# Kernel tuning notes

Hardware: AMD Instinct MI355X
Metric: run time of the kernel (lower is better)

The kernel has to match this reference:

```python
import jax, jax.numpy as jnp
import numpy as np

NH, KVH, HD = 32, 8, 128          # num heads, kv heads, head dim
HIDDEN = NH * HD                   # 4096
K_BITS = V_BITS = 4
GROUP = 32                         # quantization group size
THETA = 10000.0
FEAT = 32 // K_BITS                # values packed per int32


def _rope_cos_sin(pos, dtype=jnp.float32):
    inv_freq = 1.0 / (THETA ** (jnp.arange(0, HD, 2, dtype=jnp.float32) / HD))
    freqs = pos.astype(jnp.float32)[:, None] * inv_freq[None, :]
    emb = jnp.concatenate([freqs, freqs], axis=-1)  # [t, HD]
    return jnp.cos(emb).astype(dtype), jnp.sin(emb).astype(dtype)


def _rotate_half(x):
    x1, x2 = jnp.split(x, 2, axis=-1)
    return jnp.concatenate([-x2, x1], axis=-1)


def _apply_rope(x, pos):  # x: [b, h, t, d], pos: [t]
    cos, sin = _rope_cos_sin(pos, x.dtype)
    return x * cos[None, None] + _rotate_half(x) * sin[None, None]


def _unpack(packed, bits):
    # packed int32 [..., n] -> float [..., n * (32//bits)], little-endian bit fields
    feat = 32 // bits
    shifts = jnp.arange(feat, dtype=jnp.int32) * bits
    vals = (packed[..., None] >> shifts) & ((1 << bits) - 1)
    return vals.reshape(packed.shape[:-1] + (packed.shape[-1] * feat,)).astype(jnp.float32)


def _dequant(packed, scale, mn, bits, group):
    # group-wise affine dequant: x = q * scale + mn along last dim
    qv = _unpack(packed, bits)
    lead, L = qv.shape[:-1], qv.shape[-1]
    qv = qv.reshape(lead + (L // group, group))
    return (qv * scale[..., None] + mn[..., None]).reshape(lead + (L,))


def _repeat_kv(x, n):
    return jnp.repeat(x, n, axis=1)


def setup_inputs() -> dict:
    key = jax.random.key(0)
    ks = jax.random.split(key, 13)
    B, QL = 8, 8
    TQ, FULL_PAST = 3968, 56
    s = 0.02
    return {
        "hidden_states": jax.random.normal(ks[0], (B, QL, HIDDEN), jnp.float32),
        "Wq": jax.random.normal(ks[1], (NH * HD, HIDDEN), jnp.float32) * s,
        "Wk": jax.random.normal(ks[2], (KVH * HD, HIDDEN), jnp.float32) * s,
        "Wv": jax.random.normal(ks[3], (KVH * HD, HIDDEN), jnp.float32) * s,
        "Wo": jax.random.normal(ks[4], (NH * HD, NH * HD), jnp.float32) * s,
        "key_quant_trans": jax.random.randint(ks[5], (B, KVH, HD, TQ // FEAT), 0, 2**31 - 1, jnp.int32),
        "key_scale_trans": jax.random.uniform(ks[6], (B, KVH, HD, TQ // GROUP), jnp.float32) * 0.05 + 0.01,
        "key_mn_trans": jax.random.normal(ks[7], (B, KVH, HD, TQ // GROUP), jnp.float32) * 0.1,
        "key_full_past": jax.random.normal(ks[8], (B, KVH, FULL_PAST, HD), jnp.float32),
        "value_quant": jax.random.randint(ks[9], (B, KVH, TQ, HD // FEAT), 0, 2**31 - 1, jnp.int32),
        "value_scale": jax.random.uniform(ks[10], (B, KVH, TQ, HD // GROUP), jnp.float32) * 0.05 + 0.01,
        "value_mn": jax.random.normal(ks[11], (B, KVH, TQ, HD // GROUP), jnp.float32) * 0.1,
        "value_full_past": jax.random.normal(ks[12], (B, KVH, FULL_PAST, HD), jnp.float32),
    }


def reference(hidden_states, Wq, Wk, Wv, Wo,
              key_quant_trans, key_scale_trans, key_mn_trans, key_full_past,
              value_quant, value_scale, value_mn, value_full_past):
    b, q_len, _ = hidden_states.shape
    groups = NH // KVH
    # projections
    q = (hidden_states @ Wq.T).reshape(b, q_len, NH, HD).transpose(0, 2, 1, 3)
    k = (hidden_states @ Wk.T).reshape(b, q_len, KVH, HD).transpose(0, 2, 1, 3)
    v = (hidden_states @ Wv.T).reshape(b, q_len, KVH, HD).transpose(0, 2, 1, 3)

    TQ = key_quant_trans.shape[-1] * FEAT
    past_len = TQ + key_full_past.shape[2]
    pos_new = jnp.arange(past_len, past_len + q_len)
    qr = _apply_rope(q, pos_new)

    # quantized key segment: dequant (stored transposed [b,kvh,HD,TQ]) + fused RoPE + bmm
    kq = _dequant(key_quant_trans, key_scale_trans, key_mn_trans, K_BITS, GROUP)
    kq = _apply_rope(kq.transpose(0, 1, 3, 2), jnp.arange(TQ))  # [b,kvh,TQ,HD]
    att_quant = jnp.einsum('bhqd,bhkd->bhqk', qr, _repeat_kv(kq, groups))

    # full-precision residual key segment
    k_full = jnp.concatenate([key_full_past, k], axis=2)
    pos_full = jnp.arange(past_len + q_len - k_full.shape[2], past_len + q_len)
    k_full = _apply_rope(k_full, pos_full)
    att_full = jnp.einsum('bhqd,bhkd->bhqk', qr, _repeat_kv(k_full, groups))

    attn = jnp.concatenate([att_quant, att_full], axis=-1) / np.sqrt(HD).astype(np.float32)
    attn = jax.nn.softmax(attn.astype(jnp.float32), axis=-1).astype(qr.dtype)

    # quantized values (packed along head_dim) + full residual values
    vq = _dequant(value_quant, value_scale, value_mn, V_BITS, GROUP)  # [b,kvh,TQ,HD]
    v_full = jnp.concatenate([value_full_past, v], axis=2)
    Lf = v_full.shape[2]
    out = jnp.einsum('bhqk,bhkd->bhqd', attn[..., :-Lf], _repeat_kv(vq, groups)) \
        + jnp.einsum('bhqk,bhkd->bhqd', attn[..., -Lf:], _repeat_kv(v_full, groups))

    out = out.transpose(0, 2, 1, 3).reshape(b, q_len, NH * HD)
    return out @ Wo.T
```

## Files before the change

kernel.cpp:

```cpp
#include <hip/hip_runtime.h>

typedef unsigned short u16;
typedef short bf16x8 __attribute__((ext_vector_type(8)));
typedef float f32x4 __attribute__((ext_vector_type(4)));

__device__ __forceinline__ float b2f(u16 u){ return __uint_as_float(((unsigned)u)<<16); }
__device__ __forceinline__ u16 f2bf(float f){ return (u16)((__float_as_uint(f)+0x8000u)>>16); }
__device__ __forceinline__ float ldf(const void* p, int i, bool isbf){
  return isbf ? b2f(((const u16*)p)[i]) : ((const float*)p)[i];
}
__device__ __forceinline__ void ld8(u16* dst, const void* p, int i, bool isbf){
  if (isbf) { *(uint4*)dst = *(const uint4*)((const u16*)p + i); }
  else {
    float4 a = *(const float4*)((const float*)p + i);
    float4 b = *(const float4*)((const float*)p + i + 4);
    dst[0]=f2bf(a.x); dst[1]=f2bf(a.y); dst[2]=f2bf(a.z); dst[3]=f2bf(a.w);
    dst[4]=f2bf(b.x); dst[5]=f2bf(b.y); dst[6]=f2bf(b.z); dst[7]=f2bf(b.w);
  }
}
__device__ __forceinline__ float c8(const float* __restrict__ p, int i, int stride){
  float s = 0.f;
  #pragma unroll
  for (int k = 0; k < 8; k++) s += p[i + k*stride];
  return s;
}
#define MFMA16(a,b,c) __builtin_amdgcn_mfma_f32_16x16x32_bf16((a),(b),(c),0,0,0)

__global__ __launch_bounds__(256) void ctab_kernel(const u16* __restrict__ h,
                                                   int* __restrict__ flag,
                                                   float2* __restrict__ ctab) {
  int tid = threadIdx.x;
  if (blockIdx.x == 0) {
    int cnt = 0;
    for (int i = tid; i < 4096; i += 256) {
      int e = (h[i] >> 7) & 0xFF;
      cnt += (e >= 116 && e <= 132) ? 1 : 0;
    }
    __shared__ int sh[256];
    sh[tid] = cnt; __syncthreads();
    for (int s = 128; s > 0; s >>= 1) { if (tid < s) sh[tid] += sh[tid + s]; __syncthreads(); }
    if (tid == 0) flag[0] = (sh[0] >= 3100) ? 1 : 0;
  }
  int idx = blockIdx.x * 256 + tid;
  int dm = idx & 63, t = idx >> 6;
  float f = exp2f(-(float)dm * (13.287712379549449f / 64.0f));
  float ang = (float)t * f;
  float s, c;
  sincosf(ang, &s, &c);
  ctab[idx] = make_float2(c, s);
}

__global__ __launch_bounds__(256) void proj_kernel(
    const void* __restrict__ X, const void* __restrict__ Wa,
    const void* __restrict__ Wb, const void* __restrict__ Wc,
    float* __restrict__ out32, int Na, int Nb, int ostride,
    const int* __restrict__ flagp, int x_dyn)
{
  bool fbf = (*flagp != 0);
  bool xbf = x_dyn ? fbf : true;
  int n0 = blockIdx.x * 32;
  int ks0 = blockIdx.y * 512;
  const void* W; int wr0;
  if (n0 < Na)           { W = Wa; wr0 = n0; }
  else if (n0 < Na + Nb) { W = Wb; wr0 = n0 - Na; }
  else                   { W = Wc; wr0 = n0 - Na - Nb; }

  __shared__ u16 Xs[64][136];
  __shared__ u16 Ws[32][136];
  int tid = threadIdx.x;
  int wv = tid >> 6, lane = tid & 63, lr = lane & 15, lq = lane >> 4;
  f32x4 acc0 = {0.f,0.f,0.f,0.f}, acc1 = {0.f,0.f,0.f,0.f};

  for (int ki = 0; ki < 4; ki++) {
    int k0 = ks0 + ki * 128;
    __syncthreads();
    for (int u = tid; u < 1024; u += 256) {
      int row = u >> 4, cc = u & 15;
      ld8(&Xs[row][cc * 8], X, row * 4096 + k0 + cc * 8, xbf);
    }
    for (int u = tid; u < 512; u += 256) {
      int row = u >> 4, cc = u & 15;
      ld8(&Ws[row][cc * 8], W, (wr0 + row) * 4096 + k0 + cc * 8, fbf);
    }
    __syncthreads();
    #pragma unroll
    for (int ks = 0; ks < 4; ks++) {
      bf16x8 af = *(const bf16x8*)&Xs[wv * 16 + lr][ks * 32 + lq * 8];
      bf16x8 b0 = *(const bf16x8*)&Ws[lr][ks * 32 + lq * 8];
      bf16x8 b1 = *(const bf16x8*)&Ws[16 + lr][ks * 32 + lq * 8];
      acc0 = MFMA16(af, b0, acc0);
      acc1 = MFMA16(af, b1, acc1);
    }
  }
  float* outp = out32 + (size_t)blockIdx.y * 64 * ostride;
  #pragma unroll
  for (int r = 0; r < 4; r++) {
    outp[(wv * 16 + lq * 4 + r) * ostride + n0 + lr]      = acc0[r];
    outp[(wv * 16 + lq * 4 + r) * ostride + n0 + 16 + lr] = acc1[r];
  }
}

__global__ __launch_bounds__(256) void prep_kernel(
    const float* __restrict__ Cq32, const void* __restrict__ kfp, const void* __restrict__ vfp,
    const float2* __restrict__ ctab, const int* __restrict__ flagp,
    u16* __restrict__ qrb, u16* __restrict__ kfullb, u16* __restrict__ vfullT)
{
  bool isbf = (*flagp != 0);
  int idx = blockIdx.x * 256 + threadIdx.x;
  if (idx < 262144) {
    int d = idx & 127, row = (idx >> 7) & 31, bh = idx >> 12;
    int b = bh >> 3, kvh = bh & 7, g = row >> 3, qp = row & 7;
    int tok = b * 8 + qp, h = kvh * 4 + g;
    float x  = c8(Cq32, tok * 6144 + h * 128 + d, 393216);
    float x2 = c8(Cq32, tok * 6144 + h * 128 + (d ^ 64), 393216);
    float2 cs = ctab[(4024 + qp) * 64 + (d & 63)];
    float sgn = (d < 64) ? -1.f : 1.f;
    qrb[idx] = f2bf(x * cs.x + sgn * (x2 * cs.y));
  } else if (idx < 786432) {
    int j = idx - 262144;
    int d = j & 127, t = (j >> 7) & 63, bh = j >> 13;
    int b = bh >> 3, kvh = bh & 7;
    float x, x2;
    if (t < 56) {
      x  = ldf(kfp, (bh * 56 + t) * 128 + d, isbf);
      x2 = ldf(kfp, (bh * 56 + t) * 128 + (d ^ 64), isbf);
    } else {
      int tok = b * 8 + (t - 56);
      x  = c8(Cq32, tok * 6144 + 4096 + kvh * 128 + d, 393216);
      x2 = c8(Cq32, tok * 6144 + 4096 + kvh * 128 + (d ^ 64), 393216);
    }
    float2 cs = ctab[(3968 + t) * 64 + (d & 63)];
    float sgn = (d < 64) ? -1.f : 1.f;
    kfullb[j] = f2bf(x * cs.x + sgn * (x2 * cs.y));
  } else {
    int j = idx - 786432;
    int t = j & 63, d = (j >> 6) & 127, bh = j >> 13;
    int b = bh >> 3, kvh = bh & 7;
    float x;
    if (t < 56) x = ldf(vfp, (bh * 56 + t) * 128 + d, isbf);
    else        x = c8(Cq32, (b * 8 + t - 56) * 6144 + 5120 + kvh * 128 + d, 393216);
    vfullT[j] = f2bf(x);
  }
}

__global__ __launch_bounds__(256) void attn_kernel(
    const int* __restrict__ kqw, const void* __restrict__ ksc, const void* __restrict__ kmn,
    const int* __restrict__ vqw, const void* __restrict__ vsc, const void* __restrict__ vmn,
    const u16* __restrict__ qrb, const u16* __restrict__ kfullb, const u16* __restrict__ vfullT,
    const float2* __restrict__ ctab, const int* __restrict__ flagp,
    u16* __restrict__ Opart, float* __restrict__ ml)
{
  bool isbf = (*flagp != 0);
  int bh = blockIdx.x, grp = blockIdx.y;
  int tid = threadIdx.x;

  __shared__ __align__(16) unsigned char L[31232];
  u16 (*Ktile)[136] = (u16(*)[136])L;
  u16 (*Vtile)[72]  = (u16(*)[72])L;
  unsigned* rawK = (unsigned*)(L + 18432);
  float* sK  = (float*)(L + 23040);
  float* sKm = (float*)(L + 24576);
  unsigned* rawV = (unsigned*)(L + 18432);
  float* sV  = (float*)(L + 22784);
  float* sVm = (float*)(L + 24064);
  u16 (*Pl)[72] = (u16(*)[72])(L + 26112);
  float* pmax = (float*)(L + 30720);
  float* psum = (float*)(L + 30976);

  int wv = tid >> 6, lane = tid & 63, lr = lane & 15, lq = lane >> 4;
  int mt = wv & 1, nh = wv >> 1;

  bf16x8 qa[4];
  #pragma unroll
  for (int ks = 0; ks < 4; ks++)
    qa[ks] = *(const bf16x8*)&qrb[(bh * 32 + mt * 16 + lr) * 128 + ks * 32 + lq * 8];

  float m_prev[4], l_run[4];
  #pragma unroll
  for (int r = 0; r < 4; r++) { m_prev[r] = -INFINITY; l_run[r] = 0.f; }
  f32x4 zf = {0.f,0.f,0.f,0.f};
  f32x4 oacc[4] = {zf, zf, zf, zf};

  for (int j = 0; j < 2; j++) {
    int c = grp * 2 + j;
    if (c >= 63) break;
    bool fullc = (c == 62);

    if (!fullc) {
      #pragma unroll
      for (int it = 0; it < 4; it++) {
        int idx = tid + 256 * it;
        int d = idx >> 3, w = idx & 7;
        rawK[d * 9 + w] = (unsigned)kqw[(bh * 128 + d) * 496 + c * 8 + w];
      }
      { int d = tid >> 1, gi = tid & 1;
        sK[d * 3 + gi]  = ldf(ksc, (bh * 128 + d) * 124 + c * 2 + gi, isbf);
        sKm[d * 3 + gi] = ldf(kmn, (bh * 128 + d) * 124 + c * 2 + gi, isbf); }
    }
    __syncthreads();
    if (!fullc) {
      #pragma unroll
      for (int it = 0; it < 4; it++) {
        int idx = tid + 256 * it;
        int d = idx & 127, w = idx >> 7;
        unsigned w1 = rawK[d * 9 + w];
        unsigned w2 = rawK[(d ^ 64) * 9 + w];
        int gi = w >> 2;
        float sc1 = sK[d * 3 + gi],        m1 = sKm[d * 3 + gi];
        float sc2 = sK[(d ^ 64) * 3 + gi], m2 = sKm[(d ^ 64) * 3 + gi];
        int dm = d & 63;
        float sgn = (d < 64) ? -1.f : 1.f;
        const float2* ct = &ctab[(c * 64 + w * 8) * 64 + dm];
        #pragma unroll
        for (int i = 0; i < 8; i++) {
          float v1 = (float)((w1 >> (4 * i)) & 15u) * sc1 + m1;
          float v2 = (float)((w2 >> (4 * i)) & 15u) * sc2 + m2;
          float2 cs = ct[i * 64];
          Ktile[w * 8 + i][d] = f2bf(v1 * cs.x + sgn * (v2 * cs.y));
        }
      }
    } else {
      for (int u = tid; u < 1024; u += 256) {
        int row = u >> 4, cc = u & 15;
        *(uint4*)&Ktile[row][cc * 8] = *(const uint4*)&kfullb[(bh * 64 + row) * 128 + cc * 8];
      }
    }
    __syncthreads();
    f32x4 sacc[2] = {zf, zf};
    #pragma unroll
    for (int ks = 0; ks < 4; ks++) {
      #pragma unroll
      for (int nt = 0; nt < 2; nt++) {
        bf16x8 bfr = *(const bf16x8*)&Ktile[nh * 32 + nt * 16 + lr][ks * 32 + lq * 8];
        sacc[nt] = MFMA16(qa[ks], bfr, sacc[nt]);
      }
    }
    float mx[4];
    #pragma unroll
    for (int r = 0; r < 4; r++) {
      sacc[0][r] *= 0.08838834764831845f;
      sacc[1][r] *= 0.08838834764831845f;
      mx[r] = fmaxf(sacc[0][r], sacc[1][r]);
    }
    #pragma unroll
    for (int m = 1; m < 16; m <<= 1) {
      #pragma unroll
      for (int r = 0; r < 4; r++) mx[r] = fmaxf(mx[r], __shfl_xor(mx[r], m));
    }
    if (lr == 0) {
      #pragma unroll
      for (int r = 0; r < 4; r++) pmax[wv * 16 + lq * 4 + r] = mx[r];
    }
    __syncthreads();
    if (!fullc) {
      #pragma unroll
      for (int it = 0; it < 4; it++) {
        int idx = tid + 256 * it;
        int t = idx >> 4, w = idx & 15;
        rawV[t * 17 + w] = (unsigned)vqw[(bh * 3968 + c * 64 + t) * 16 + w];
      }
      { int t = tid >> 2, gq = tid & 3;
        sV[t * 5 + gq]  = ldf(vsc, (bh * 3968 + c * 64 + t) * 4 + gq, isbf);
        sVm[t * 5 + gq] = ldf(vmn, (bh * 3968 + c * 64 + t) * 4 + gq, isbf); }
    } else {
      for (int u = tid; u < 1024; u += 256) {
        int d = u >> 3, t8 = u & 7;
        *(uint4*)&Vtile[d][t8 * 8] = *(const uint4*)&vfullT[(bh * 128 + d) * 64 + t8 * 8];
      }
    }
    float alpha[4], osum[4];
    #pragma unroll
    for (int r = 0; r < 4; r++) {
      float cm = fmaxf(mx[r], pmax[(wv ^ 2) * 16 + lq * 4 + r]);
      float mn2 = fmaxf(m_prev[r], cm);
      alpha[r] = __expf(m_prev[r] - mn2);
      m_prev[r] = mn2;
    }
    u16 pb[2][4];
    #pragma unroll
    for (int r = 0; r < 4; r++) {
      float p0 = __expf(sacc[0][r] - m_prev[r]);
      float p1 = __expf(sacc[1][r] - m_prev[r]);
      pb[0][r] = f2bf(p0); pb[1][r] = f2bf(p1);
      osum[r] = b2f(pb[0][r]) + b2f(pb[1][r]);
    }
    #pragma unroll
    for (int m = 1; m < 16; m <<= 1) {
      #pragma unroll
      for (int r = 0; r < 4; r++) osum[r] += __shfl_xor(osum[r], m);
    }
    #pragma unroll
    for (int nt = 0; nt < 2; nt++)
      #pragma unroll
      for (int r = 0; r < 4; r++)
        Pl[mt * 16 + lq * 4 + r][nh * 32 + nt * 16 + lr] = pb[nt][r];
    if (lr == 0) {
      #pragma unroll
      for (int r = 0; r < 4; r++) psum[wv * 16 + lq * 4 + r] = osum[r];
    }
    __syncthreads();
    if (!fullc) {
      #pragma unroll
      for (int it = 0; it < 4; it++) {
        int idx = tid + 256 * it;
        int tl = idx & 63, w = idx >> 6;
        unsigned wd = rawV[tl * 17 + w];
        int gq = w >> 2;
        float sc = sV[tl * 5 + gq], mn = sVm[tl * 5 + gq];
        #pragma unroll
        for (int i = 0; i < 8; i++)
          Vtile[w * 8 + i][tl] = f2bf((float)((wd >> (4 * i)) & 15u) * sc + mn);
      }
    }
    #pragma unroll
    for (int r = 0; r < 4; r++)
      l_run[r] = l_run[r] * alpha[r] + osum[r] + psum[(wv ^ 2) * 16 + lq * 4 + r];
    __syncthreads();
    f32x4 pv[4] = {zf, zf, zf, zf};
    #pragma unroll
    for (int ks = 0; ks < 2; ks++) {
      bf16x8 af = *(const bf16x8*)&Pl[mt * 16 + lr][ks * 32 + lq * 8];
      #pragma unroll
      for (int nt = 0; nt < 4; nt++) {
        bf16x8 bfr = *(const bf16x8*)&Vtile[nh * 64 + nt * 16 + lr][ks * 32 + lq * 8];
        pv[nt] = MFMA16(af, bfr, pv[nt]);
      }
    }
    #pragma unroll
    for (int nt = 0; nt < 4; nt++)
      #pragma unroll
      for (int r = 0; r < 4; r++)
        oacc[nt][r] = oacc[nt][r] * alpha[r] + pv[nt][r];
  }

  u16* Ob = Opart + (size_t)((bh * 32 + grp) * 32) * 128;
  #pragma unroll
  for (int nt = 0; nt < 4; nt++)
    #pragma unroll
    for (int r = 0; r < 4; r++)
      Ob[(mt * 16 + lq * 4 + r) * 128 + nh * 64 + nt * 16 + lr] = f2bf(oacc[nt][r]);
  if (wv < 2 && lr == 0) {
    #pragma unroll
    for (int r = 0; r < 4; r++) {
      ml[((bh * 32 + grp) * 32 + mt * 16 + lq * 4 + r) * 2 + 0] = m_prev[r];
      ml[((bh * 32 + grp) * 32 + mt * 16 + lq * 4 + r) * 2 + 1] = l_run[r];
    }
  }
}

__global__ __launch_bounds__(256) void combine_kernel(
    const u16* __restrict__ Opart, const float* __restrict__ ml, u16* __restrict__ attn_out)
{
  int bh = blockIdx.x, dq = blockIdx.y, tid = threadIdx.x;
  __shared__ float Wg[32][33];
  __shared__ float Ls[32];
  if (tid < 32) {
    int row = tid;
    float M = -INFINITY;
    for (int g = 0; g < 32; g++)
      M = fmaxf(M, ml[((bh * 32 + g) * 32 + row) * 2]);
    float Lacc = 0.f;
    for (int g = 0; g < 32; g++) {
      float m = ml[((bh * 32 + g) * 32 + row) * 2];
      float l = ml[((bh * 32 + g) * 32 + row) * 2 + 1];
      float w = __expf(m - M);
      Wg[g][row] = w;
      Lacc += l * w;
    }
    Ls[row] = Lacc;
  }
  __syncthreads();
  int row = tid >> 3, ds = tid & 7;
  int d0 = dq * 32 + ds * 4;
  float a0 = 0.f, a1 = 0.f, a2 = 0.f, a3 = 0.f;
  for (int g = 0; g < 32; g++) {
    float w = Wg[g][row];
    const u16* p = Opart + (size_t)((bh * 32 + g) * 32 + row) * 128 + d0;
    uint2 v = *(const uint2*)p;
    const u16* h = (const u16*)&v;
    a0 += w * b2f(h[0]); a1 += w * b2f(h[1]); a2 += w * b2f(h[2]); a3 += w * b2f(h[3]);
  }
  float inv = 1.0f / Ls[row];
  int b = bh >> 3, kvh = bh & 7, hg = row >> 3, qp = row & 7;
  u16* dst = attn_out + (size_t)(b * 8 + qp) * 4096 + (kvh * 4 + hg) * 128 + d0;
  dst[0] = f2bf(a0 * inv); dst[1] = f2bf(a1 * inv);
  dst[2] = f2bf(a2 * inv); dst[3] = f2bf(a3 * inv);
}

__global__ __launch_bounds__(256) void cast_kernel(
    const float* __restrict__ O32, const int* __restrict__ flagp, void* __restrict__ out)
{
  int i = blockIdx.x * 256 + threadIdx.x;
  float v = c8(O32, i, 262144);
  if (*flagp) ((u16*)out)[i] = f2bf(v);
  else        ((float*)out)[i] = v;
}

extern "C" void kernel_launch(void* const* d_in, const int* in_sizes, int n_in,
                              void* d_out, int out_size, void* d_ws, size_t ws_size,
                              hipStream_t stream)
{
  const void* hidden = d_in[0];
  const void* Wq  = d_in[1];
  const void* Wk  = d_in[2];
  const void* Wv  = d_in[3];
  const void* Wo  = d_in[4];
  const int*  kqw = (const int*)d_in[5];
  const void* ksc = d_in[6];
  const void* kmn = d_in[7];
  const void* kfp = d_in[8];
  const int*  vqw = (const int*)d_in[9];
  const void* vsc = d_in[10];
  const void* vmn = d_in[11];
  const void* vfp = d_in[12];

  char* ws = (char*)d_ws;
  int*    flag     = (int*)(ws);
  float2* ctab     = (float2*)(ws + 256);
  float*  Cq32     = (float*)(ws + 2064640);
  u16*    Opart    = (u16*)(ws + 2064640);
  float*  O32      = (float*)(ws + 2064640);
  u16*    qrb      = (u16*)(ws + 18841856);
  u16*    attn_out = qrb;
  u16*    kfullb   = (u16*)(ws + 19366144);
  u16*    vfullT   = (u16*)(ws + 20414720);
  float*  ml       = (float*)(ws + 21463296);

  ctab_kernel<<<1008, 256, 0, stream>>>((const u16*)hidden, flag, ctab);
  proj_kernel<<<dim3(192, 8), 256, 0, stream>>>(hidden, Wq, Wk, Wv, Cq32, 4096, 1024, 6144, flag, 1);
  prep_kernel<<<5120, 256, 0, stream>>>(Cq32, kfp, vfp, ctab, flag, qrb, kfullb, vfullT);
  attn_kernel<<<dim3(64, 32), 256, 0, stream>>>(kqw, ksc, kmn, vqw, vsc, vmn,
                                                qrb, kfullb, vfullT, ctab, flag, Opart, ml);
  combine_kernel<<<dim3(64, 4), 256, 0, stream>>>(Opart, ml, attn_out);
  proj_kernel<<<dim3(128, 8), 256, 0, stream>>>(attn_out, Wo, Wo, Wo, O32, 4096, 0, 4096, flag, 0);
  cast_kernel<<<1024, 256, 0, stream>>>(O32, flag, d_out);
}
```

Before: 317.2 us.

## Prefetch quantized K/V chunks into registers and dequantize directly, fewer splits

The attention kernel no longer stages raw packed K/V words and scales in shared memory. Each thread loads its packed words and scales for the next chunk into registers while the current chunk is processed, then dequantizes straight into the tiles. Barriers are replaced by a lighter waitcnt plus s_barrier, and one barrier and one LDS staging phase per chunk are dropped. The split count drops from 32 to 16 groups, each handling 4 chunks, which shrinks the combine work but halves grid parallelism and adds register pressure.

```diff
diff --git a/kernel.cpp b/kernel.cpp
--- a/kernel.cpp
+++ b/kernel.cpp
@@ -8,6 +8,11 @@
 __device__ __forceinline__ u16 f2bf(float f){ return (u16)((__float_as_uint(f)+0x8000u)>>16); }
 __device__ __forceinline__ float ldf(const void* p, int i, bool isbf){
   return isbf ? b2f(((const u16*)p)[i]) : ((const float*)p)[i];
+}
+__device__ __forceinline__ float2 ld2(const void* p, int i, bool isbf){
+  if (isbf) { unsigned u = *(const unsigned*)((const u16*)p + i);
+              return make_float2(b2f((u16)(u & 0xffffu)), b2f((u16)(u >> 16))); }
+  return *(const float2*)((const float*)p + i);
 }
 __device__ __forceinline__ void ld8(u16* dst, const void* p, int i, bool isbf){
   if (isbf) { *(uint4*)dst = *(const uint4*)((const u16*)p + i); }
@@ -24,6 +29,7 @@
   for (int k = 0; k < 8; k++) s += p[i + k*stride];
   return s;
 }
+__device__ __forceinline__ void bar(){ asm volatile("s_waitcnt lgkmcnt(0)\n\ts_barrier" ::: "memory"); }
 #define MFMA16(a,b,c) __builtin_amdgcn_mfma_f32_16x16x32_bf16((a),(b),(c),0,0,0)
 
 __global__ __launch_bounds__(256) void ctab_kernel(const u16* __restrict__ h,
@@ -154,26 +160,41 @@
   int bh = blockIdx.x, grp = blockIdx.y;
   int tid = threadIdx.x;
 
-  __shared__ __align__(16) unsigned char L[31232];
+  __shared__ __align__(16) unsigned char L[23552];
   u16 (*Ktile)[136] = (u16(*)[136])L;
   u16 (*Vtile)[72]  = (u16(*)[72])L;
-  unsigned* rawK = (unsigned*)(L + 18432);
-  float* sK  = (float*)(L + 23040);
-  float* sKm = (float*)(L + 24576);
-  unsigned* rawV = (unsigned*)(L + 18432);
-  float* sV  = (float*)(L + 22784);
-  float* sVm = (float*)(L + 24064);
-  u16 (*Pl)[72] = (u16(*)[72])(L + 26112);
-  float* pmax = (float*)(L + 30720);
-  float* psum = (float*)(L + 30976);
+  u16 (*Pl)[72] = (u16(*)[72])(L + 18432);
+  float* pmax = (float*)(L + 23040);
+  float* psum = (float*)(L + 23296);
 
   int wv = tid >> 6, lane = tid & 63, lr = lane & 15, lq = lane >> 4;
   int mt = wv & 1, nh = wv >> 1;
+
+  const int* kq_lo = kqw + (bh * 128 + lane) * 496;
+  const int* kq_hi = kq_lo + 64 * 496;
+  int klo = (bh * 128 + lane) * 124;
+  int khi = klo + 64 * 124;
+  const int* vqp = vqw + (bh * 3968 + lane) * 16 + wv * 4;
+  int voff = (bh * 3968 + lane) * 4 + wv;
 
   bf16x8 qa[4];
   #pragma unroll
   for (int ks = 0; ks < 4; ks++)
     qa[ks] = *(const bf16x8*)&qrb[(bh * 32 + mt * 16 + lr) * 128 + ks * 32 + lq * 8];
+
+  unsigned kwl[2], kwh[2];
+  float2 ksl, kml, ksh, kmh;
+  uint4 vw;
+  float vs, vm;
+  {
+    int c0 = grp * 4;
+    kwl[0] = kq_lo[c0 * 8 + wv]; kwl[1] = kq_lo[c0 * 8 + wv + 4];
+    kwh[0] = kq_hi[c0 * 8 + wv]; kwh[1] = kq_hi[c0 * 8 + wv + 4];
+    ksl = ld2(ksc, klo + c0 * 2, isbf); kml = ld2(kmn, klo + c0 * 2, isbf);
+    ksh = ld2(ksc, khi + c0 * 2, isbf); kmh = ld2(kmn, khi + c0 * 2, isbf);
+    vw = *(const uint4*)(vqp + c0 * 1024);
+    vs = ldf(vsc, voff + c0 * 256, isbf); vm = ldf(vmn, voff + c0 * 256, isbf);
+  }
 
   float m_prev[4], l_run[4];
   #pragma unroll
@@ -181,42 +202,28 @@
   f32x4 zf = {0.f,0.f,0.f,0.f};
   f32x4 oacc[4] = {zf, zf, zf, zf};
 
-  for (int j = 0; j < 2; j++) {
-    int c = grp * 2 + j;
+  for (int j = 0; j < 4; j++) {
+    int c = grp * 4 + j;
     if (c >= 63) break;
     bool fullc = (c == 62);
-
+    bool pf = (j < 3) && (c + 1 < 62);
+
+    bar();
     if (!fullc) {
       #pragma unroll
-      for (int it = 0; it < 4; it++) {
-        int idx = tid + 256 * it;
-        int d = idx >> 3, w = idx & 7;
-        rawK[d * 9 + w] = (unsigned)kqw[(bh * 128 + d) * 496 + c * 8 + w];
-      }
-      { int d = tid >> 1, gi = tid & 1;
-        sK[d * 3 + gi]  = ldf(ksc, (bh * 128 + d) * 124 + c * 2 + gi, isbf);
-        sKm[d * 3 + gi] = ldf(kmn, (bh * 128 + d) * 124 + c * 2 + gi, isbf); }
-    }
-    __syncthreads();
-    if (!fullc) {
-      #pragma unroll
-      for (int it = 0; it < 4; it++) {
-        int idx = tid + 256 * it;
-        int d = idx & 127, w = idx >> 7;
-        unsigned w1 = rawK[d * 9 + w];
-        unsigned w2 = rawK[(d ^ 64) * 9 + w];
-        int gi = w >> 2;
-        float sc1 = sK[d * 3 + gi],        m1 = sKm[d * 3 + gi];
-        float sc2 = sK[(d ^ 64) * 3 + gi], m2 = sKm[(d ^ 64) * 3 + gi];
-        int dm = d & 63;
-        float sgn = (d < 64) ? -1.f : 1.f;
-        const float2* ct = &ctab[(c * 64 + w * 8) * 64 + dm];
+      for (int it = 0; it < 2; it++) {
+        int w = wv + 4 * it;
+        unsigned w1 = kwl[it], w2 = kwh[it];
+        float sc1 = it ? ksl.y : ksl.x, m1 = it ? kml.y : kml.x;
+        float sc2 = it ? ksh.y : ksh.x, m2 = it ? kmh.y : kmh.x;
+        const float2* ct = &ctab[(c * 64 + w * 8) * 64 + lane];
         #pragma unroll
         for (int i = 0; i < 8; i++) {
           float v1 = (float)((w1 >> (4 * i)) & 15u) * sc1 + m1;
           float v2 = (float)((w2 >> (4 * i)) & 15u) * sc2 + m2;
           float2 cs = ct[i * 64];
-          Ktile[w * 8 + i][d] = f2bf(v1 * cs.x + sgn * (v2 * cs.y));
+          Ktile[w * 8 + i][lane]      = f2bf(v1 * cs.x - v2 * cs.y);
+          Ktile[w * 8 + i][lane + 64] = f2bf(v2 * cs.x + v1 * cs.y);
         }
       }
     } else {
@@ -225,7 +232,14 @@
         *(uint4*)&Ktile[row][cc * 8] = *(const uint4*)&kfullb[(bh * 64 + row) * 128 + cc * 8];
       }
     }
-    __syncthreads();
+    if (pf) {
+      int cn = c + 1;
+      kwl[0] = kq_lo[cn * 8 + wv]; kwl[1] = kq_lo[cn * 8 + wv + 4];
+      kwh[0] = kq_hi[cn * 8 + wv]; kwh[1] = kq_hi[cn * 8 + wv + 4];
+      ksl = ld2(ksc, klo + cn * 2, isbf); kml = ld2(kmn, klo + cn * 2, isbf);
+      ksh = ld2(ksc, khi + cn * 2, isbf); kmh = ld2(kmn, khi + cn * 2, isbf);
+    }
+    bar();
     f32x4 sacc[2] = {zf, zf};
     #pragma unroll
     for (int ks = 0; ks < 4; ks++) {
@@ -251,22 +265,27 @@
       #pragma unroll
       for (int r = 0; r < 4; r++) pmax[wv * 16 + lq * 4 + r] = mx[r];
     }
-    __syncthreads();
+    bar();
     if (!fullc) {
+      unsigned wds[4] = {vw.x, vw.y, vw.z, vw.w};
       #pragma unroll
       for (int it = 0; it < 4; it++) {
-        int idx = tid + 256 * it;
-        int t = idx >> 4, w = idx & 15;
-        rawV[t * 17 + w] = (unsigned)vqw[(bh * 3968 + c * 64 + t) * 16 + w];
-      }
-      { int t = tid >> 2, gq = tid & 3;
-        sV[t * 5 + gq]  = ldf(vsc, (bh * 3968 + c * 64 + t) * 4 + gq, isbf);
-        sVm[t * 5 + gq] = ldf(vmn, (bh * 3968 + c * 64 + t) * 4 + gq, isbf); }
+        int w = wv * 4 + it;
+        unsigned wd = wds[it];
+        #pragma unroll
+        for (int i = 0; i < 8; i++)
+          Vtile[w * 8 + i][lane] = f2bf((float)((wd >> (4 * i)) & 15u) * vs + vm);
+      }
     } else {
       for (int u = tid; u < 1024; u += 256) {
-        int d = u >> 3, t8 = u & 7;
-        *(uint4*)&Vtile[d][t8 * 8] = *(const uint4*)&vfullT[(bh * 128 + d) * 64 + t8 * 8];
-      }
+        int dd = u >> 3, t8 = u & 7;
+        *(uint4*)&Vtile[dd][t8 * 8] = *(const uint4*)&vfullT[(bh * 128 + dd) * 64 + t8 * 8];
+      }
+    }
+    if (pf) {
+      int cn = c + 1;
+      vw = *(const uint4*)(vqp + cn * 1024);
+      vs = ldf(vsc, voff + cn * 256, isbf); vm = ldf(vmn, voff + cn * 256, isbf);
     }
     float alpha[4], osum[4];
     #pragma unroll
@@ -298,24 +317,7 @@
       #pragma unroll
       for (int r = 0; r < 4; r++) psum[wv * 16 + lq * 4 + r] = osum[r];
     }
-    __syncthreads();
-    if (!fullc) {
-      #pragma unroll
-      for (int it = 0; it < 4; it++) {
-        int idx = tid + 256 * it;
-        int tl = idx & 63, w = idx >> 6;
-        unsigned wd = rawV[tl * 17 + w];
-        int gq = w >> 2;
-        float sc = sV[tl * 5 + gq], mn = sVm[tl * 5 + gq];
-        #pragma unroll
-        for (int i = 0; i < 8; i++)
-          Vtile[w * 8 + i][tl] = f2bf((float)((wd >> (4 * i)) & 15u) * sc + mn);
-      }
-    }
-    #pragma unroll
-    for (int r = 0; r < 4; r++)
-      l_run[r] = l_run[r] * alpha[r] + osum[r] + psum[(wv ^ 2) * 16 + lq * 4 + r];
-    __syncthreads();
+    bar();
     f32x4 pv[4] = {zf, zf, zf, zf};
     #pragma unroll
     for (int ks = 0; ks < 2; ks++) {
@@ -327,13 +329,16 @@
       }
     }
     #pragma unroll
+    for (int r = 0; r < 4; r++)
+      l_run[r] = l_run[r] * alpha[r] + osum[r] + psum[(wv ^ 2) * 16 + lq * 4 + r];
+    #pragma unroll
     for (int nt = 0; nt < 4; nt++)
       #pragma unroll
       for (int r = 0; r < 4; r++)
         oacc[nt][r] = oacc[nt][r] * alpha[r] + pv[nt][r];
   }
 
-  u16* Ob = Opart + (size_t)((bh * 32 + grp) * 32) * 128;
+  u16* Ob = Opart + (size_t)((bh * 16 + grp) * 32) * 128;
   #pragma unroll
   for (int nt = 0; nt < 4; nt++)
     #pragma unroll
@@ -342,8 +347,8 @@
   if (wv < 2 && lr == 0) {
     #pragma unroll
     for (int r = 0; r < 4; r++) {
-      ml[((bh * 32 + grp) * 32 + mt * 16 + lq * 4 + r) * 2 + 0] = m_prev[r];
-      ml[((bh * 32 + grp) * 32 + mt * 16 + lq * 4 + r) * 2 + 1] = l_run[r];
+      ml[((bh * 16 + grp) * 32 + mt * 16 + lq * 4 + r) * 2 + 0] = m_prev[r];
+      ml[((bh * 16 + grp) * 32 + mt * 16 + lq * 4 + r) * 2 + 1] = l_run[r];
     }
   }
 }
@@ -352,17 +357,17 @@
     const u16* __restrict__ Opart, const float* __restrict__ ml, u16* __restrict__ attn_out)
 {
   int bh = blockIdx.x, dq = blockIdx.y, tid = threadIdx.x;
-  __shared__ float Wg[32][33];
+  __shared__ float Wg[16][33];
   __shared__ float Ls[32];
   if (tid < 32) {
     int row = tid;
     float M = -INFINITY;
-    for (int g = 0; g < 32; g++)
-      M = fmaxf(M, ml[((bh * 32 + g) * 32 + row) * 2]);
+    for (int g = 0; g < 16; g++)
+      M = fmaxf(M, ml[((bh * 16 + g) * 32 + row) * 2]);
     float Lacc = 0.f;
-    for (int g = 0; g < 32; g++) {
-      float m = ml[((bh * 32 + g) * 32 + row) * 2];
-      float l = ml[((bh * 32 + g) * 32 + row) * 2 + 1];
+    for (int g = 0; g < 16; g++) {
+      float m = ml[((bh * 16 + g) * 32 + row) * 2];
+      float l = ml[((bh * 16 + g) * 32 + row) * 2 + 1];
       float w = __expf(m - M);
       Wg[g][row] = w;
       Lacc += l * w;
@@ -373,9 +378,9 @@
   int row = tid >> 3, ds = tid & 7;
   int d0 = dq * 32 + ds * 4;
   float a0 = 0.f, a1 = 0.f, a2 = 0.f, a3 = 0.f;
-  for (int g = 0; g < 32; g++) {
+  for (int g = 0; g < 16; g++) {
     float w = Wg[g][row];
-    const u16* p = Opart + (size_t)((bh * 32 + g) * 32 + row) * 128 + d0;
+    const u16* p = Opart + (size_t)((bh * 16 + g) * 32 + row) * 128 + d0;
     uint2 v = *(const uint2*)p;
     const u16* h = (const u16*)&v;
     a0 += w * b2f(h[0]); a1 += w * b2f(h[1]); a2 += w * b2f(h[2]); a3 += w * b2f(h[3]);
@@ -429,7 +434,7 @@
   ctab_kernel<<<1008, 256, 0, stream>>>((const u16*)hidden, flag, ctab);
   proj_kernel<<<dim3(192, 8), 256, 0, stream>>>(hidden, Wq, Wk, Wv, Cq32, 4096, 1024, 6144, flag, 1);
   prep_kernel<<<5120, 256, 0, stream>>>(Cq32, kfp, vfp, ctab, flag, qrb, kfullb, vfullT);
-  attn_kernel<<<dim3(64, 32), 256, 0, stream>>>(kqw, ksc, kmn, vqw, vsc, vmn,
+  attn_kernel<<<dim3(64, 16), 256, 0, stream>>>(kqw, ksc, kmn, vqw, vsc, vmn,
                                                 qrb, kfullb, vfullT, ctab, flag, Opart, ml);
   combine_kernel<<<dim3(64, 4), 256, 0, stream>>>(Opart, ml, attn_out);
   proj_kernel<<<dim3(128, 8), 256, 0, stream>>>(attn_out, Wo, Wo, Wo, O32, 4096, 0, 4096, flag, 0);
```

Result: no change. 316.9 us (-0.1%).
